# Optimization experiments

Hardware: AMD Instinct MI355X
Metric: run time of the kernel (lower is better)

## Reference

```python
import jax, jax.numpy as jnp
import numpy as np

B, S, H = 256, 1, 2048
Q_SIZE = 4096        # num_heads * head_dim = 32 * 128
QKV = 4 * H          # expected_linear_qkv = 8192
K_SZ = 4             # conv kernel size
C = 32               # ssm channels
WSCALE = 0.02


def setup_inputs() -> dict:
    key = jax.random.key(0)
    ks = jax.random.split(key, 13)
    return {
        "hidden_states": jax.random.normal(ks[0], (B, S, H), jnp.float32),
        "W_qkv": jax.random.normal(ks[1], (QKV, H), jnp.float32) * WSCALE,
        "b_qkv": jax.random.normal(ks[2], (QKV,), jnp.float32) * WSCALE,
        "W_gate": jax.random.normal(ks[3], (2 * H, H), jnp.float32) * WSCALE,
        "W_alpha": jax.random.normal(ks[4], (C, H), jnp.float32) * WSCALE,
        "W_beta": jax.random.normal(ks[5], (C, H), jnp.float32) * WSCALE,
        "W_out": jax.random.normal(ks[6], (H, 2 * H), jnp.float32) * WSCALE,
        "ssm_state_a": jax.random.normal(ks[7], (C,), jnp.float32),
        "ssm_dt_bias": jax.random.normal(ks[8], (C,), jnp.float32),
        "ssm_norm_weight": jnp.ones((128,), jnp.float32),
        "conv_kernel": jax.random.normal(ks[9], (QKV, K_SZ), jnp.float32) * WSCALE,
        "ssm_state": jax.random.normal(ks[10], (B, C), jnp.float32),
        "conv_state": jax.random.normal(ks[11], (B, K_SZ, QKV), jnp.float32),
    }


def reference(hidden_states, W_qkv, b_qkv, W_gate, W_alpha, W_beta, W_out,
              ssm_state_a, ssm_dt_bias, ssm_norm_weight, conv_kernel,
              ssm_state, conv_state):
    bsz = hidden_states.shape[0]
    # qkv projection (decode: only last token matters downstream)
    qkv = jnp.einsum('bsh,dh->bsd', hidden_states, W_qkv) + b_qkv  # [B,S,4H]
    mixed_qkv = qkv[:, -1, :].astype(jnp.float32)                  # [B,4H]
    hidden_last = hidden_states[:, -1, :]                          # [B,H]

    # roll conv state and append current token, then causal conv1d step
    cs = jnp.concatenate([conv_state[:, 1:, :], mixed_qkv[:, None, :]], axis=1)  # [B,K,4H]
    conv_out = jnp.einsum('bkd,dk->bd', cs, conv_kernel)           # [B,4H]

    target_size = conv_out.shape[-1] - Q_SIZE                      # 2H = 4096
    k_size = target_size // 2                                      # 2048
    core_base = conv_out[:, Q_SIZE:]                               # [B,2H]
    k_proj = core_base[:, :k_size]
    v_proj = core_base[:, k_size:]

    # alpha/beta gating of the SSM state
    a = hidden_last @ W_alpha.T                                    # [B,C]
    b = hidden_last @ W_beta.T                                     # [B,C]
    g = -jnp.exp(ssm_state_a)[None, :] * jax.nn.softplus(a + ssm_dt_bias[None, :])
    beta = jax.nn.sigmoid(b)

    group_width = k_size // C                                      # 64
    v_group = v_proj[:, :group_width * C].reshape(bsz, C, group_width).mean(-1)
    k_group = k_proj[:, :group_width * C].reshape(bsz, C, group_width).mean(-1)

    new_state = jnp.exp(g) * ssm_state + beta * v_group            # [B,C]
    state_signal = new_state * jax.nn.sigmoid(k_group)             # [B,C]

    repeat_factor = target_size // C                               # 128
    expanded = jnp.repeat(state_signal, repeat_factor, axis=-1)[:, :target_size]

    core = core_base + expanded
    core = core * jax.lax.rsqrt(jnp.mean(core * core, axis=-1, keepdims=True) + 1e-6)
    gate = jax.nn.sigmoid(hidden_last @ W_gate.T).astype(jnp.float32)
    core = core * gate * jnp.mean(ssm_norm_weight)
    core = core.astype(hidden_states.dtype)

    out = (core @ W_out.T)[:, None, :]                             # [B,1,H]
    return out
```

## Files before the change

kernel.cpp:

```cpp
#include <hip/hip_runtime.h>
#include <hip/hip_bf16.h>
#include <stdint.h>

#define BSZ 256
#define NQ 4096
#define N1 8320
#define K1 2048
#define N3 2048
#define K3 4096

typedef __attribute__((ext_vector_type(8))) short bf16x8;
typedef __attribute__((ext_vector_type(4))) float f32x4;

__device__ __forceinline__ unsigned short f2bf(float f) {
  union { float f; unsigned u; } v; v.f = f;
  unsigned r = v.u + 0x7fffu + ((v.u >> 16) & 1u);
  return (unsigned short)(r >> 16);
}

__device__ __forceinline__ bf16x8 pack8(float4 a, float4 b) {
  union { bf16x8 v; unsigned short u[8]; } o;
  o.u[0] = f2bf(a.x); o.u[1] = f2bf(a.y); o.u[2] = f2bf(a.z); o.u[3] = f2bf(a.w);
  o.u[4] = f2bf(b.x); o.u[5] = f2bf(b.y); o.u[6] = f2bf(b.z); o.u[7] = f2bf(b.w);
  return o.v;
}

__device__ __forceinline__ void gload_lds16(const void* g, void* lds_uniform) {
  __builtin_amdgcn_global_load_lds(
      (const __attribute__((address_space(1))) unsigned int*)g,
      (__attribute__((address_space(3))) unsigned int*)lds_uniform, 16, 0, 0);
}

__global__ __launch_bounds__(256) void cvt_kernel(const float* __restrict__ x,
                                                  unsigned short* __restrict__ y) {
  int i = (blockIdx.x * 256 + threadIdx.x) * 8;
  float4 a = *(const float4*)(x + i);
  float4 b = *(const float4*)(x + i + 4);
  ushort4 o0 = { f2bf(a.x), f2bf(a.y), f2bf(a.z), f2bf(a.w) };
  ushort4 o1 = { f2bf(b.x), f2bf(b.y), f2bf(b.z), f2bf(b.w) };
  *(ushort4*)(y + i) = o0;
  *(ushort4*)(y + i + 4) = o1;
}

__global__ __launch_bounds__(256) void gemm1_kernel(
    const unsigned short* __restrict__ A16,
    const float* __restrict__ Wqkv, const float* __restrict__ Wgate,
    const float* __restrict__ Walpha, const float* __restrict__ Wbeta,
    float* __restrict__ P) {
  __shared__ unsigned short sA[2][128 * 32];
  __shared__ unsigned short sB[2][64 * 32];
  const int tid = threadIdx.x, lane = tid & 63, wv = tid >> 6;
  const int wr = wv >> 1, wc = wv & 1;
  const int rt = blockIdx.x * 128;
  const int n0 = blockIdx.y * 64;
  const int kb = blockIdx.z * 1024;

  const int brow = tid >> 2, bcol = (tid & 3) * 8;
  const float* bsrc;
  {
    int n = n0 + brow;
    const float* s;
    if (n < 4096)       s = Wqkv  + (size_t)(4096 + n) * K1;
    else if (n < 8192)  s = Wgate + (size_t)(n - 4096) * K1;
    else if (n < 8224)  s = Walpha + (size_t)(n - 8192) * K1;
    else if (n < 8256)  s = Wbeta + (size_t)(n - 8224) * K1;
    else                s = Walpha;
    bsrc = s + kb + bcol;
  }
  const char* asrc0 = (const char*)(A16 + (size_t)(rt + (tid >> 2)) * K1 + kb) + (tid & 3) * 16;
  const char* asrc1 = asrc0 + (size_t)64 * K1 * 2;

  f32x4 acc[4][2];
#pragma unroll
  for (int i = 0; i < 4; i++)
#pragma unroll
    for (int j = 0; j < 2; j++) { f32x4 z = {0.f, 0.f, 0.f, 0.f}; acc[i][j] = z; }

  float4 pb0, pb1;
  gload_lds16(asrc0, (char*)sA[0] + wv * 1024);
  gload_lds16(asrc1, (char*)sA[0] + 4096 + wv * 1024);
  pb0 = *(const float4*)bsrc;
  pb1 = *(const float4*)(bsrc + 4);
  *(bf16x8*)&sB[0][brow * 32 + bcol] = pack8(pb0, pb1);

  for (int ks = 0; ks < 32; ks++) {
    const int cur = ks & 1, nxt = cur ^ 1;
    __syncthreads();
    if (ks + 1 < 32) {
      gload_lds16(asrc0 + (ks + 1) * 64, (char*)sA[nxt] + wv * 1024);
      gload_lds16(asrc1 + (ks + 1) * 64, (char*)sA[nxt] + 4096 + wv * 1024);
      pb0 = *(const float4*)(bsrc + (ks + 1) * 32);
      pb1 = *(const float4*)(bsrc + (ks + 1) * 32 + 4);
    }
    bf16x8 aF[4], bF[2];
#pragma unroll
    for (int i = 0; i < 4; i++)
      aF[i] = *(const bf16x8*)(&sA[cur][(wr * 64 + i * 16 + (lane & 15)) * 32 + (lane >> 4) * 8]);
#pragma unroll
    for (int j = 0; j < 2; j++)
      bF[j] = *(const bf16x8*)(&sB[cur][(wc * 32 + j * 16 + (lane & 15)) * 32 + (lane >> 4) * 8]);
#pragma unroll
    for (int i = 0; i < 4; i++)
#pragma unroll
      for (int j = 0; j < 2; j++)
        acc[i][j] = __builtin_amdgcn_mfma_f32_16x16x32_bf16(aF[i], bF[j], acc[i][j], 0, 0, 0);
    if (ks + 1 < 32)
      *(bf16x8*)&sB[nxt][brow * 32 + bcol] = pack8(pb0, pb1);
  }

#pragma unroll
  for (int i = 0; i < 4; i++) {
    int row = rt + wr * 64 + i * 16 + (lane >> 4) * 4;
#pragma unroll
    for (int j = 0; j < 2; j++) {
      int col = n0 + wc * 32 + j * 16 + (lane & 15);
#pragma unroll
      for (int r = 0; r < 4; r++)
        atomicAdd(&P[(size_t)(row + r) * N1 + col], acc[i][j][r]);
    }
  }
}

__global__ __launch_bounds__(512) void fuse_kernel(
    const float* __restrict__ P,
    const float* __restrict__ bqkv,
    const float* __restrict__ ck,
    const float* __restrict__ cstate,
    const float* __restrict__ ssa,
    const float* __restrict__ dtb,
    const float* __restrict__ nw,
    const float* __restrict__ sstate,
    unsigned short* __restrict__ C16) {
  __shared__ __align__(16) float cb[4096];
  __shared__ float gsum[64];
  __shared__ float ssl[32];
  __shared__ float red[16];
  const int b = blockIdx.x, tid = threadIdx.x;
  const int lane = tid & 63, wv = tid >> 6;
  const float* Pb = P + (size_t)b * N1;

  if (wv == 0) {
    float m = nw[lane] + nw[lane + 64];
#pragma unroll
    for (int off = 32; off; off >>= 1) m += __shfl_down(m, off, 64);
    if (lane == 0) red[8] = m * (1.f / 128.f);
  }

#pragma unroll
  for (int it = 0; it < 2; it++) {
    int j = (it * 512 + tid) * 4;
    float4 q  = *(const float4*)(Pb + j);
    float4 bq = *(const float4*)(bqkv + NQ + j);
    float mqx = q.x + bq.x, mqy = q.y + bq.y, mqz = q.z + bq.z, mqw = q.w + bq.w;
    const float* csb = cstate + (size_t)b * 4 * 8192 + NQ + j;
    float4 c1 = *(const float4*)(csb + 8192);
    float4 c2 = *(const float4*)(csb + 16384);
    float4 c3 = *(const float4*)(csb + 24576);
    float4 k0v = *(const float4*)(ck + (size_t)(NQ + j) * 4);
    float4 k1v = *(const float4*)(ck + (size_t)(NQ + j + 1) * 4);
    float4 k2v = *(const float4*)(ck + (size_t)(NQ + j + 2) * 4);
    float4 k3v = *(const float4*)(ck + (size_t)(NQ + j + 3) * 4);
    float4 cbv;
    cbv.x = c1.x * k0v.x + c2.x * k0v.y + c3.x * k0v.z + mqx * k0v.w;
    cbv.y = c1.y * k1v.x + c2.y * k1v.y + c3.y * k1v.z + mqy * k1v.w;
    cbv.z = c1.z * k2v.x + c2.z * k2v.y + c3.z * k2v.z + mqz * k2v.w;
    cbv.w = c1.w * k3v.x + c2.w * k3v.y + c3.w * k3v.z + mqw * k3v.w;
    *(float4*)(cb + j) = cbv;
    float s = cbv.x + cbv.y + cbv.z + cbv.w;
    s += __shfl_xor(s, 1, 64); s += __shfl_xor(s, 2, 64);
    s += __shfl_xor(s, 4, 64); s += __shfl_xor(s, 8, 64);
    if ((lane & 15) == 0) gsum[(it * 512 + tid) >> 4] = s;
  }
  __syncthreads();

  if (tid < 32) {
    float a  = Pb[8192 + tid];
    float bc = Pb[8224 + tid];
    float kg = gsum[tid] * (1.f / 64.f);
    float vg = gsum[32 + tid] * (1.f / 64.f);
    float x = a + dtb[tid];
    float sp = fmaxf(x, 0.f) + log1pf(expf(-fabsf(x)));
    float g = -expf(ssa[tid]) * sp;
    float beta = 1.f / (1.f + expf(-bc));
    float ns = expf(g) * sstate[b * 32 + tid] + beta * vg;
    ssl[tid] = ns / (1.f + expf(-kg));
  }
  __syncthreads();

  float sq = 0.f;
  float4 c1r[2];
#pragma unroll
  for (int it = 0; it < 2; it++) {
    int j = (it * 512 + tid) * 4;
    float4 v = *(const float4*)(cb + j);
    float sv = ssl[j >> 7];
    v.x += sv; v.y += sv; v.z += sv; v.w += sv;
    c1r[it] = v;
    sq += v.x * v.x + v.y * v.y + v.z * v.z + v.w * v.w;
  }
#pragma unroll
  for (int off = 32; off; off >>= 1) sq += __shfl_down(sq, off, 64);
  if (lane == 0) red[wv] = sq;
  __syncthreads();
  if (tid == 0) {
    float t = red[0] + red[1] + red[2] + red[3] + red[4] + red[5] + red[6] + red[7];
    red[9] = rsqrtf(t * (1.f / 4096.f) + 1e-6f);
  }
  __syncthreads();
  float rms = red[9], mwv = red[8];

#pragma unroll
  for (int it = 0; it < 2; it++) {
    int j = (it * 512 + tid) * 4;
    float4 g0 = *(const float4*)(Pb + NQ + j);
    float4 v = c1r[it];
    float ox = v.x * rms * mwv / (1.f + expf(-g0.x));
    float oy = v.y * rms * mwv / (1.f + expf(-g0.y));
    float oz = v.z * rms * mwv / (1.f + expf(-g0.z));
    float ow = v.w * rms * mwv / (1.f + expf(-g0.w));
    ushort4 u = { f2bf(ox), f2bf(oy), f2bf(oz), f2bf(ow) };
    *(ushort4*)(C16 + (size_t)b * 4096 + j) = u;
  }
}

__global__ __launch_bounds__(256) void gemm3_kernel(
    const unsigned short* __restrict__ A16,
    const float* __restrict__ Wout,
    float* __restrict__ out) {
  __shared__ unsigned short sA[2][128 * 32];
  __shared__ unsigned short sB[2][64 * 32];
  const int tid = threadIdx.x, lane = tid & 63, wv = tid >> 6;
  const int wr = wv >> 1, wc = wv & 1;
  const int rt = blockIdx.x * 128;
  const int n0 = blockIdx.y * 64;
  const int kb = blockIdx.z * 512;

  const int brow = tid >> 2, bcol = (tid & 3) * 8;
  const float* bsrc = Wout + (size_t)(n0 + brow) * K3 + kb + bcol;
  const char* asrc0 = (const char*)(A16 + (size_t)(rt + (tid >> 2)) * K3 + kb) + (tid & 3) * 16;
  const char* asrc1 = asrc0 + (size_t)64 * K3 * 2;

  f32x4 acc[4][2];
#pragma unroll
  for (int i = 0; i < 4; i++)
#pragma unroll
    for (int j = 0; j < 2; j++) { f32x4 z = {0.f, 0.f, 0.f, 0.f}; acc[i][j] = z; }

  float4 pb0, pb1;
  gload_lds16(asrc0, (char*)sA[0] + wv * 1024);
  gload_lds16(asrc1, (char*)sA[0] + 4096 + wv * 1024);
  pb0 = *(const float4*)bsrc;
  pb1 = *(const float4*)(bsrc + 4);
  *(bf16x8*)&sB[0][brow * 32 + bcol] = pack8(pb0, pb1);

  for (int ks = 0; ks < 16; ks++) {
    const int cur = ks & 1, nxt = cur ^ 1;
    __syncthreads();
    if (ks + 1 < 16) {
      gload_lds16(asrc0 + (ks + 1) * 64, (char*)sA[nxt] + wv * 1024);
      gload_lds16(asrc1 + (ks + 1) * 64, (char*)sA[nxt] + 4096 + wv * 1024);
      pb0 = *(const float4*)(bsrc + (ks + 1) * 32);
      pb1 = *(const float4*)(bsrc + (ks + 1) * 32 + 4);
    }
    bf16x8 aF[4], bF[2];
#pragma unroll
    for (int i = 0; i < 4; i++)
      aF[i] = *(const bf16x8*)(&sA[cur][(wr * 64 + i * 16 + (lane & 15)) * 32 + (lane >> 4) * 8]);
#pragma unroll
    for (int j = 0; j < 2; j++)
      bF[j] = *(const bf16x8*)(&sB[cur][(wc * 32 + j * 16 + (lane & 15)) * 32 + (lane >> 4) * 8]);
#pragma unroll
    for (int i = 0; i < 4; i++)
#pragma unroll
      for (int j = 0; j < 2; j++)
        acc[i][j] = __builtin_amdgcn_mfma_f32_16x16x32_bf16(aF[i], bF[j], acc[i][j], 0, 0, 0);
    if (ks + 1 < 16)
      *(bf16x8*)&sB[nxt][brow * 32 + bcol] = pack8(pb0, pb1);
  }

#pragma unroll
  for (int i = 0; i < 4; i++) {
    int row = rt + wr * 64 + i * 16 + (lane >> 4) * 4;
#pragma unroll
    for (int j = 0; j < 2; j++) {
      int col = n0 + wc * 32 + j * 16 + (lane & 15);
#pragma unroll
      for (int r = 0; r < 4; r++)
        atomicAdd(&out[(size_t)(row + r) * N3 + col], acc[i][j][r]);
    }
  }
}

extern "C" void kernel_launch(void* const* d_in, const int* in_sizes, int n_in,
                              void* d_out, int out_size, void* d_ws, size_t ws_size,
                              hipStream_t stream) {
  const float* hidden = (const float*)d_in[0];
  const float* Wqkv   = (const float*)d_in[1];
  const float* bqkv   = (const float*)d_in[2];
  const float* Wgate  = (const float*)d_in[3];
  const float* Walpha = (const float*)d_in[4];
  const float* Wbeta  = (const float*)d_in[5];
  const float* Wout   = (const float*)d_in[6];
  const float* ssa    = (const float*)d_in[7];
  const float* dtb    = (const float*)d_in[8];
  const float* nw     = (const float*)d_in[9];
  const float* ck     = (const float*)d_in[10];
  const float* sstate = (const float*)d_in[11];
  const float* cstate = (const float*)d_in[12];
  float* out = (float*)d_out;

  char* ws = (char*)d_ws;
  unsigned short* A16 = (unsigned short*)ws;
  float* P = (float*)(ws + (1 << 20));
  unsigned short* C16 = (unsigned short*)(ws + (1 << 20) + 8519680);

  hipMemsetAsync(d_out, 0, (size_t)BSZ * N3 * sizeof(float), stream);
  hipMemsetAsync(P, 0, (size_t)BSZ * N1 * sizeof(float), stream);
  cvt_kernel<<<256, 256, 0, stream>>>(hidden, A16);
  gemm1_kernel<<<dim3(2, 130, 2), 256, 0, stream>>>(A16, Wqkv, Wgate, Walpha, Wbeta, P);
  fuse_kernel<<<256, 512, 0, stream>>>(P, bqkv, ck, cstate, ssa, dtb, nw, sstate, C16);
  gemm3_kernel<<<dim3(2, 32, 8), 256, 0, stream>>>(C16, Wout, out);
}
```

Before: 248.2 us.

## Load GEMM operands directly to registers and replace split-K atomics with partial buffers

Both GEMM kernels drop LDS staging and barriers. Each lane now loads its MFMA fragments straight from global memory into registers, with a one-step register prefetch and a 2-blocks-per-CU launch bound. Split-K atomicAdd is replaced by plain stores into per-split partial buffers, summed in the fuse kernel and a new reduce kernel, which also removes the two memsets. The cost is extra workspace, more global traffic, and possible redundant or uncoalesced fragment loads, since neighbouring warps no longer share tiles through LDS.

```diff
diff --git a/kernel.cpp b/kernel.cpp
--- a/kernel.cpp
+++ b/kernel.cpp
@@ -23,12 +23,6 @@
   o.u[0] = f2bf(a.x); o.u[1] = f2bf(a.y); o.u[2] = f2bf(a.z); o.u[3] = f2bf(a.w);
   o.u[4] = f2bf(b.x); o.u[5] = f2bf(b.y); o.u[6] = f2bf(b.z); o.u[7] = f2bf(b.w);
   return o.v;
-}
-
-__device__ __forceinline__ void gload_lds16(const void* g, void* lds_uniform) {
-  __builtin_amdgcn_global_load_lds(
-      (const __attribute__((address_space(1))) unsigned int*)g,
-      (__attribute__((address_space(3))) unsigned int*)lds_uniform, 16, 0, 0);
 }
 
 __global__ __launch_bounds__(256) void cvt_kernel(const float* __restrict__ x,
@@ -42,33 +36,34 @@
   *(ushort4*)(y + i + 4) = o1;
 }
 
-__global__ __launch_bounds__(256) void gemm1_kernel(
+__global__ __launch_bounds__(256, 2) void gemm1_kernel(
     const unsigned short* __restrict__ A16,
     const float* __restrict__ Wqkv, const float* __restrict__ Wgate,
     const float* __restrict__ Walpha, const float* __restrict__ Wbeta,
     float* __restrict__ P) {
-  __shared__ unsigned short sA[2][128 * 32];
-  __shared__ unsigned short sB[2][64 * 32];
   const int tid = threadIdx.x, lane = tid & 63, wv = tid >> 6;
   const int wr = wv >> 1, wc = wv & 1;
   const int rt = blockIdx.x * 128;
   const int n0 = blockIdx.y * 64;
   const int kb = blockIdx.z * 1024;
-
-  const int brow = tid >> 2, bcol = (tid & 3) * 8;
-  const float* bsrc;
-  {
-    int n = n0 + brow;
+  const int l15 = lane & 15, lk = (lane >> 4) * 8;
+
+  const unsigned short* aptr[4];
+#pragma unroll
+  for (int i = 0; i < 4; i++)
+    aptr[i] = A16 + (size_t)(rt + wr * 64 + i * 16 + l15) * K1 + kb + lk;
+  const float* bptr[2];
+#pragma unroll
+  for (int j = 0; j < 2; j++) {
+    int n = n0 + wc * 32 + j * 16 + l15;
     const float* s;
     if (n < 4096)       s = Wqkv  + (size_t)(4096 + n) * K1;
     else if (n < 8192)  s = Wgate + (size_t)(n - 4096) * K1;
     else if (n < 8224)  s = Walpha + (size_t)(n - 8192) * K1;
     else if (n < 8256)  s = Wbeta + (size_t)(n - 8224) * K1;
     else                s = Walpha;
-    bsrc = s + kb + bcol;
-  }
-  const char* asrc0 = (const char*)(A16 + (size_t)(rt + (tid >> 2)) * K1 + kb) + (tid & 3) * 16;
-  const char* asrc1 = asrc0 + (size_t)64 * K1 * 2;
+    bptr[j] = s + kb + lk;
+  }
 
   f32x4 acc[4][2];
 #pragma unroll
@@ -76,47 +71,51 @@
 #pragma unroll
     for (int j = 0; j < 2; j++) { f32x4 z = {0.f, 0.f, 0.f, 0.f}; acc[i][j] = z; }
 
-  float4 pb0, pb1;
-  gload_lds16(asrc0, (char*)sA[0] + wv * 1024);
-  gload_lds16(asrc1, (char*)sA[0] + 4096 + wv * 1024);
-  pb0 = *(const float4*)bsrc;
-  pb1 = *(const float4*)(bsrc + 4);
-  *(bf16x8*)&sB[0][brow * 32 + bcol] = pack8(pb0, pb1);
-
+  bf16x8 aC[4]; float4 bC[2][2];
+#pragma unroll
+  for (int i = 0; i < 4; i++) aC[i] = *(const bf16x8*)(aptr[i]);
+#pragma unroll
+  for (int j = 0; j < 2; j++) {
+    bC[j][0] = *(const float4*)(bptr[j]);
+    bC[j][1] = *(const float4*)(bptr[j] + 4);
+  }
+
+#pragma unroll 2
   for (int ks = 0; ks < 32; ks++) {
-    const int cur = ks & 1, nxt = cur ^ 1;
-    __syncthreads();
+    bf16x8 aN[4]; float4 bN[2][2];
     if (ks + 1 < 32) {
-      gload_lds16(asrc0 + (ks + 1) * 64, (char*)sA[nxt] + wv * 1024);
-      gload_lds16(asrc1 + (ks + 1) * 64, (char*)sA[nxt] + 4096 + wv * 1024);
-      pb0 = *(const float4*)(bsrc + (ks + 1) * 32);
-      pb1 = *(const float4*)(bsrc + (ks + 1) * 32 + 4);
+#pragma unroll
+      for (int i = 0; i < 4; i++) aN[i] = *(const bf16x8*)(aptr[i] + (ks + 1) * 32);
+#pragma unroll
+      for (int j = 0; j < 2; j++) {
+        bN[j][0] = *(const float4*)(bptr[j] + (ks + 1) * 32);
+        bN[j][1] = *(const float4*)(bptr[j] + (ks + 1) * 32 + 4);
+      }
     }
-    bf16x8 aF[4], bF[2];
+    bf16x8 bFr[2];
+#pragma unroll
+    for (int j = 0; j < 2; j++) bFr[j] = pack8(bC[j][0], bC[j][1]);
 #pragma unroll
     for (int i = 0; i < 4; i++)
-      aF[i] = *(const bf16x8*)(&sA[cur][(wr * 64 + i * 16 + (lane & 15)) * 32 + (lane >> 4) * 8]);
-#pragma unroll
-    for (int j = 0; j < 2; j++)
-      bF[j] = *(const bf16x8*)(&sB[cur][(wc * 32 + j * 16 + (lane & 15)) * 32 + (lane >> 4) * 8]);
-#pragma unroll
-    for (int i = 0; i < 4; i++)
 #pragma unroll
       for (int j = 0; j < 2; j++)
-        acc[i][j] = __builtin_amdgcn_mfma_f32_16x16x32_bf16(aF[i], bF[j], acc[i][j], 0, 0, 0);
-    if (ks + 1 < 32)
-      *(bf16x8*)&sB[nxt][brow * 32 + bcol] = pack8(pb0, pb1);
-  }
-
+        acc[i][j] = __builtin_amdgcn_mfma_f32_16x16x32_bf16(aC[i], bFr[j], acc[i][j], 0, 0, 0);
+#pragma unroll
+    for (int i = 0; i < 4; i++) aC[i] = aN[i];
+#pragma unroll
+    for (int j = 0; j < 2; j++) { bC[j][0] = bN[j][0]; bC[j][1] = bN[j][1]; }
+  }
+
+  float* Pz = P + (size_t)blockIdx.z * ((size_t)BSZ * N1);
 #pragma unroll
   for (int i = 0; i < 4; i++) {
     int row = rt + wr * 64 + i * 16 + (lane >> 4) * 4;
 #pragma unroll
     for (int j = 0; j < 2; j++) {
-      int col = n0 + wc * 32 + j * 16 + (lane & 15);
+      int col = n0 + wc * 32 + j * 16 + l15;
 #pragma unroll
       for (int r = 0; r < 4; r++)
-        atomicAdd(&P[(size_t)(row + r) * N1 + col], acc[i][j][r]);
+        Pz[(size_t)(row + r) * N1 + col] = acc[i][j][r];
     }
   }
 }
@@ -137,7 +136,8 @@
   __shared__ float red[16];
   const int b = blockIdx.x, tid = threadIdx.x;
   const int lane = tid & 63, wv = tid >> 6;
-  const float* Pb = P + (size_t)b * N1;
+  const float* P0 = P + (size_t)b * N1;
+  const float* P1 = P + (size_t)(BSZ + b) * N1;
 
   if (wv == 0) {
     float m = nw[lane] + nw[lane + 64];
@@ -149,9 +149,11 @@
 #pragma unroll
   for (int it = 0; it < 2; it++) {
     int j = (it * 512 + tid) * 4;
-    float4 q  = *(const float4*)(Pb + j);
+    float4 q0 = *(const float4*)(P0 + j);
+    float4 q1 = *(const float4*)(P1 + j);
     float4 bq = *(const float4*)(bqkv + NQ + j);
-    float mqx = q.x + bq.x, mqy = q.y + bq.y, mqz = q.z + bq.z, mqw = q.w + bq.w;
+    float mqx = q0.x + q1.x + bq.x, mqy = q0.y + q1.y + bq.y;
+    float mqz = q0.z + q1.z + bq.z, mqw = q0.w + q1.w + bq.w;
     const float* csb = cstate + (size_t)b * 4 * 8192 + NQ + j;
     float4 c1 = *(const float4*)(csb + 8192);
     float4 c2 = *(const float4*)(csb + 16384);
@@ -174,8 +176,8 @@
   __syncthreads();
 
   if (tid < 32) {
-    float a  = Pb[8192 + tid];
-    float bc = Pb[8224 + tid];
+    float a  = P0[8192 + tid] + P1[8192 + tid];
+    float bc = P0[8224 + tid] + P1[8224 + tid];
     float kg = gsum[tid] * (1.f / 64.f);
     float vg = gsum[32 + tid] * (1.f / 64.f);
     float x = a + dtb[tid];
@@ -212,33 +214,37 @@
 #pragma unroll
   for (int it = 0; it < 2; it++) {
     int j = (it * 512 + tid) * 4;
-    float4 g0 = *(const float4*)(Pb + NQ + j);
+    float4 g0x = *(const float4*)(P0 + NQ + j);
+    float4 g1x = *(const float4*)(P1 + NQ + j);
     float4 v = c1r[it];
-    float ox = v.x * rms * mwv / (1.f + expf(-g0.x));
-    float oy = v.y * rms * mwv / (1.f + expf(-g0.y));
-    float oz = v.z * rms * mwv / (1.f + expf(-g0.z));
-    float ow = v.w * rms * mwv / (1.f + expf(-g0.w));
+    float ox = v.x * rms * mwv / (1.f + expf(-(g0x.x + g1x.x)));
+    float oy = v.y * rms * mwv / (1.f + expf(-(g0x.y + g1x.y)));
+    float oz = v.z * rms * mwv / (1.f + expf(-(g0x.z + g1x.z)));
+    float ow = v.w * rms * mwv / (1.f + expf(-(g0x.w + g1x.w)));
     ushort4 u = { f2bf(ox), f2bf(oy), f2bf(oz), f2bf(ow) };
     *(ushort4*)(C16 + (size_t)b * 4096 + j) = u;
   }
 }
 
-__global__ __launch_bounds__(256) void gemm3_kernel(
+__global__ __launch_bounds__(256, 2) void gemm3_kernel(
     const unsigned short* __restrict__ A16,
     const float* __restrict__ Wout,
-    float* __restrict__ out) {
-  __shared__ unsigned short sA[2][128 * 32];
-  __shared__ unsigned short sB[2][64 * 32];
+    float* __restrict__ OP) {
   const int tid = threadIdx.x, lane = tid & 63, wv = tid >> 6;
   const int wr = wv >> 1, wc = wv & 1;
   const int rt = blockIdx.x * 128;
   const int n0 = blockIdx.y * 64;
   const int kb = blockIdx.z * 512;
-
-  const int brow = tid >> 2, bcol = (tid & 3) * 8;
-  const float* bsrc = Wout + (size_t)(n0 + brow) * K3 + kb + bcol;
-  const char* asrc0 = (const char*)(A16 + (size_t)(rt + (tid >> 2)) * K3 + kb) + (tid & 3) * 16;
-  const char* asrc1 = asrc0 + (size_t)64 * K3 * 2;
+  const int l15 = lane & 15, lk = (lane >> 4) * 8;
+
+  const unsigned short* aptr[4];
+#pragma unroll
+  for (int i = 0; i < 4; i++)
+    aptr[i] = A16 + (size_t)(rt + wr * 64 + i * 16 + l15) * K3 + kb + lk;
+  const float* bptr[2];
+#pragma unroll
+  for (int j = 0; j < 2; j++)
+    bptr[j] = Wout + (size_t)(n0 + wc * 32 + j * 16 + l15) * K3 + kb + lk;
 
   f32x4 acc[4][2];
 #pragma unroll
@@ -246,49 +252,65 @@
 #pragma unroll
     for (int j = 0; j < 2; j++) { f32x4 z = {0.f, 0.f, 0.f, 0.f}; acc[i][j] = z; }
 
-  float4 pb0, pb1;
-  gload_lds16(asrc0, (char*)sA[0] + wv * 1024);
-  gload_lds16(asrc1, (char*)sA[0] + 4096 + wv * 1024);
-  pb0 = *(const float4*)bsrc;
-  pb1 = *(const float4*)(bsrc + 4);
-  *(bf16x8*)&sB[0][brow * 32 + bcol] = pack8(pb0, pb1);
-
+  bf16x8 aC[4]; float4 bC[2][2];
+#pragma unroll
+  for (int i = 0; i < 4; i++) aC[i] = *(const bf16x8*)(aptr[i]);
+#pragma unroll
+  for (int j = 0; j < 2; j++) {
+    bC[j][0] = *(const float4*)(bptr[j]);
+    bC[j][1] = *(const float4*)(bptr[j] + 4);
+  }
+
+#pragma unroll 2
   for (int ks = 0; ks < 16; ks++) {
-    const int cur = ks & 1, nxt = cur ^ 1;
-    __syncthreads();
+    bf16x8 aN[4]; float4 bN[2][2];
     if (ks + 1 < 16) {
-      gload_lds16(asrc0 + (ks + 1) * 64, (char*)sA[nxt] + wv * 1024);
-      gload_lds16(asrc1 + (ks + 1) * 64, (char*)sA[nxt] + 4096 + wv * 1024);
-      pb0 = *(const float4*)(bsrc + (ks + 1) * 32);
-      pb1 = *(const float4*)(bsrc + (ks + 1) * 32 + 4);
+#pragma unroll
+      for (int i = 0; i < 4; i++) aN[i] = *(const bf16x8*)(aptr[i] + (ks + 1) * 32);
+#pragma unroll
+      for (int j = 0; j < 2; j++) {
+        bN[j][0] = *(const float4*)(bptr[j] + (ks + 1) * 32);
+        bN[j][1] = *(const float4*)(bptr[j] + (ks + 1) * 32 + 4);
+      }
     }
-    bf16x8 aF[4], bF[2];
+    bf16x8 bFr[2];
+#pragma unroll
+    for (int j = 0; j < 2; j++) bFr[j] = pack8(bC[j][0], bC[j][1]);
 #pragma unroll
     for (int i = 0; i < 4; i++)
-      aF[i] = *(const bf16x8*)(&sA[cur][(wr * 64 + i * 16 + (lane & 15)) * 32 + (lane >> 4) * 8]);
-#pragma unroll
-    for (int j = 0; j < 2; j++)
-      bF[j] = *(const bf16x8*)(&sB[cur][(wc * 32 + j * 16 + (lane & 15)) * 32 + (lane >> 4) * 8]);
-#pragma unroll
-    for (int i = 0; i < 4; i++)
 #pragma unroll
       for (int j = 0; j < 2; j++)
-        acc[i][j] = __builtin_amdgcn_mfma_f32_16x16x32_bf16(aF[i], bF[j], acc[i][j], 0, 0, 0);
-    if (ks + 1 < 16)
-      *(bf16x8*)&sB[nxt][brow * 32 + bcol] = pack8(pb0, pb1);
-  }
-
+        acc[i][j] = __builtin_amdgcn_mfma_f32_16x16x32_bf16(aC[i], bFr[j], acc[i][j], 0, 0, 0);
+#pragma unroll
+    for (int i = 0; i < 4; i++) aC[i] = aN[i];
+#pragma unroll
+    for (int j = 0; j < 2; j++) { bC[j][0] = bN[j][0]; bC[j][1] = bN[j][1]; }
+  }
+
+  float* Oz = OP + (size_t)blockIdx.z * ((size_t)BSZ * N3);
 #pragma unroll
   for (int i = 0; i < 4; i++) {
     int row = rt + wr * 64 + i * 16 + (lane >> 4) * 4;
 #pragma unroll
     for (int j = 0; j < 2; j++) {
-      int col = n0 + wc * 32 + j * 16 + (lane & 15);
+      int col = n0 + wc * 32 + j * 16 + l15;
 #pragma unroll
       for (int r = 0; r < 4; r++)
-        atomicAdd(&out[(size_t)(row + r) * N3 + col], acc[i][j][r]);
+        Oz[(size_t)(row + r) * N3 + col] = acc[i][j][r];
     }
   }
+}
+
+__global__ __launch_bounds__(256) void reduce_kernel(const float* __restrict__ OP,
+                                                     float* __restrict__ out) {
+  int i = (blockIdx.x * 256 + threadIdx.x) * 4;
+  float4 s = *(const float4*)(OP + i);
+#pragma unroll
+  for (int z = 1; z < 8; z++) {
+    float4 v = *(const float4*)(OP + (size_t)z * BSZ * N3 + i);
+    s.x += v.x; s.y += v.y; s.z += v.z; s.w += v.w;
+  }
+  *(float4*)(out + i) = s;
 }
 
 extern "C" void kernel_launch(void* const* d_in, const int* in_sizes, int n_in,
@@ -311,13 +333,13 @@
 
   char* ws = (char*)d_ws;
   unsigned short* A16 = (unsigned short*)ws;
-  float* P = (float*)(ws + (1 << 20));
-  unsigned short* C16 = (unsigned short*)(ws + (1 << 20) + 8519680);
-
-  hipMemsetAsync(d_out, 0, (size_t)BSZ * N3 * sizeof(float), stream);
-  hipMemsetAsync(P, 0, (size_t)BSZ * N1 * sizeof(float), stream);
+  float* P   = (float*)(ws + (1 << 20));
+  unsigned short* C16 = (unsigned short*)(ws + (1 << 20) + 17039360);
+  float* OP  = (float*)(ws + (1 << 20) + 17039360 + (2 << 20));
+
   cvt_kernel<<<256, 256, 0, stream>>>(hidden, A16);
   gemm1_kernel<<<dim3(2, 130, 2), 256, 0, stream>>>(A16, Wqkv, Wgate, Walpha, Wbeta, P);
   fuse_kernel<<<256, 512, 0, stream>>>(P, bqkv, ck, cstate, ssa, dtb, nw, sstate, C16);
-  gemm3_kernel<<<dim3(2, 32, 8), 256, 0, stream>>>(C16, Wout, out);
-}
+  gemm3_kernel<<<dim3(2, 32, 8), 256, 0, stream>>>(C16, Wout, OP);
+  reduce_kernel<<<512, 256, 0, stream>>>(OP, out);
+}
```

Result: slower. 294.2 us (+18.5%).
